# Kernel optimization log

Measured on AMD Instinct MI355X. Metric: run time of the kernel, lower is better.

The kernel has to match this reference:

```python
import jax, jax.numpy as jnp
import numpy as np

IMG = 8       # image_size
LH = 150      # l_h
LQ = 10       # l_q
K = 10        # value-iteration steps
B = 16384     # batch
N_STATES = 2 + IMG * IMG


def _conv(x, w, pad):
    # NCHW conv, stride 1
    return jax.lax.conv_general_dilated(
        x, w, window_strides=(1, 1), padding=[(pad, pad), (pad, pad)],
        dimension_numbers=('NCHW', 'OIHW', 'NCHW'))


def setup_inputs() -> dict:
    key = jax.random.key(0)
    ks = jax.random.split(key, 8)
    grid = jax.random.normal(ks[0], (B, IMG * IMG), dtype=jnp.float32)
    pos = jax.random.randint(ks[1], (B, 2), 0, IMG).astype(jnp.float32)
    S = jnp.concatenate([grid, pos], axis=1)                      # [B, 66]
    Wh = jax.random.normal(ks[2], (LH, 1, 3, 3), jnp.float32) * 0.1
    bh = jnp.zeros((LH,), jnp.float32)
    Wr = jax.random.normal(ks[3], (1, LH, 1, 1), jnp.float32) * 0.1
    Wq = jax.random.normal(ks[4], (LQ, 1, 3, 3), jnp.float32) * 0.1
    w = jax.random.normal(ks[5], (LQ, 1, 3, 3), jnp.float32) * 0.1
    Wfc = jax.random.normal(ks[6], (8, LQ), jnp.float32) * 0.1
    return {'S': S, 'Wh': Wh, 'bh': bh, 'Wr': Wr, 'Wq': Wq, 'w': w, 'Wfc': Wfc}


def reference(S, Wh, bh, Wr, Wq, w, Wfc):
    X = S[:, :IMG * IMG].reshape(-1, 1, IMG, IMG)                 # [B,1,8,8]
    s1 = S[:, IMG * IMG].astype(jnp.int32)                        # row index
    s2 = S[:, IMG * IMG + 1].astype(jnp.int32)                    # col index

    h = _conv(X, Wh, 1) + bh[None, :, None, None]                 # [B,150,8,8]
    r = _conv(h, Wr, 0)                                           # [B,1,8,8]
    q = _conv(r, Wq, 1)                                           # [B,10,8,8]
    v = jnp.max(q, axis=1, keepdims=True)                         # [B,1,8,8]

    Wcat = jnp.concatenate([Wq, w], axis=1)                       # [10,2,3,3]

    def step(v, _):
        qq = _conv(jnp.concatenate([r, v], axis=1), Wcat, 1)
        return jnp.max(qq, axis=1, keepdims=True), None

    v, _ = jax.lax.scan(step, v, None, length=K - 1)
    q = _conv(jnp.concatenate([r, v], axis=1), Wcat, 1)           # [B,10,8,8]

    bidx = jnp.arange(q.shape[0])
    q_sel = q[bidx, :, s1, s2]                                    # [B,10]
    logits = q_sel @ Wfc.T                                        # [B,8]
    return logits
```

## Files before the change

### kernel.cpp

```cpp
#include <hip/hip_runtime.h>

#define IMG 8
#define LH 150
#define LQ 10
#define KITER 10
#define ROW (IMG * IMG + 2)

__device__ __forceinline__ float bperm(int byte_addr, float v) {
    return __builtin_bit_cast(float,
        __builtin_amdgcn_ds_bpermute(byte_addr, __builtin_bit_cast(int, v)));
}

__device__ __forceinline__ float max10(const float q[LQ]) {
    const float g0 = fmaxf(fmaxf(q[0], q[1]), q[2]);
    const float g1 = fmaxf(fmaxf(q[3], q[4]), q[5]);
    const float g2 = fmaxf(fmaxf(q[6], q[7]), q[8]);
    return fmaxf(fmaxf(g0, g1), fmaxf(g2, q[9]));
}

__global__ void weff_kernel(const float* __restrict__ Wh,
                            const float* __restrict__ bh,
                            const float* __restrict__ Wr,
                            float* __restrict__ ws) {
    const int wv = threadIdx.x >> 6;
    const int lane = threadIdx.x & 63;
    float partial = 0.f;
    for (int c = lane; c < LH; c += 64) {
        const float wr = Wr[c];
        partial += wr * ((wv < 9) ? Wh[c * 9 + wv] : bh[c]);
    }
    #pragma unroll
    for (int off = 32; off > 0; off >>= 1)
        partial += __shfl_xor(partial, off);
    if (lane == 0) ws[wv] = partial;
}

__global__ __launch_bounds__(256, 2) void vin_kernel(
    const float* __restrict__ S,
    const float* __restrict__ Wq,
    const float* __restrict__ w,
    const float* __restrict__ Wfc,
    const float* __restrict__ ws,
    float* __restrict__ out,
    int B) {
    const int wave = threadIdx.x >> 6;
    const int lane = threadIdx.x & 63;
    const long b0 = (long)(blockIdx.x * 4 + wave) * 2;
    if (b0 >= B) return;

    const int y = lane >> 3, x = lane & 7;

    int   addr[9];
    float msk[9];
    #pragma unroll
    for (int t = 0; t < 9; ++t) {
        const int dy = t / 3 - 1, dx = t % 3 - 1;
        const int ny = y + dy, nx = x + dx;
        const bool v = ((unsigned)ny < 8u) && ((unsigned)nx < 8u);
        addr[t] = (v ? (ny * 8 + nx) : 0) << 2;
        msk[t]  = v ? 1.f : 0.f;
    }

    float wreg[LQ][9];
    #pragma unroll
    for (int o = 0; o < LQ; ++o)
        #pragma unroll
        for (int t = 0; t < 9; ++t)
            wreg[o][t] = w[o * 9 + t] * msk[t];

    const float* S0 = S + b0 * ROW;
    const float X0 = S0[lane];
    const float X1 = S0[ROW + lane];
    const int sel0 = ((int)S0[IMG * IMG] * 8 + (int)S0[IMG * IMG + 1]) << 2;
    const int sel1 = ((int)S0[ROW + IMG * IMG] * 8 + (int)S0[ROW + IMG * IMG + 1]) << 2;

    float r0 = ws[9], r1 = ws[9];
    #pragma unroll
    for (int t = 0; t < 9; ++t) {
        const float wm = ws[t] * msk[t];
        r0 = fmaf(wm, bperm(addr[t], X0), r0);
        r1 = fmaf(wm, bperm(addr[t], X1), r1);
    }

    float qr0[LQ], qr1[LQ];
    #pragma unroll
    for (int t = 0; t < 9; ++t) {
        const float a0 = bperm(addr[t], r0) * msk[t];
        const float a1 = bperm(addr[t], r1) * msk[t];
        #pragma unroll
        for (int o = 0; o < LQ; ++o) {
            const float wq = Wq[o * 9 + t];
            if (t == 0) { qr0[o] = a0 * wq; qr1[o] = a1 * wq; }
            else        { qr0[o] = fmaf(a0, wq, qr0[o]);
                          qr1[o] = fmaf(a1, wq, qr1[o]); }
        }
    }

    float v0 = max10(qr0), v1 = max10(qr1);

    #pragma unroll
    for (int k = 0; k < KITER - 1; ++k) {
        float vn0[9], vn1[9];
        #pragma unroll
        for (int t = 0; t < 9; ++t) {
            vn0[t] = bperm(addr[t], v0);
            vn1[t] = bperm(addr[t], v1);
        }
        float m0, m1;
        #pragma unroll
        for (int o = 0; o < LQ; ++o) {
            float acc0 = qr0[o], acc1 = qr1[o];
            #pragma unroll
            for (int t = 0; t < 9; ++t) {
                acc0 = fmaf(vn0[t], wreg[o][t], acc0);
                acc1 = fmaf(vn1[t], wreg[o][t], acc1);
            }
            if (o == 0) { m0 = acc0; m1 = acc1; }
            else        { m0 = fmaxf(m0, acc0); m1 = fmaxf(m1, acc1); }
        }
        v0 = m0; v1 = m1;
    }

    float qs0[LQ], qs1[LQ];
    {
        float vn0[9], vn1[9];
        #pragma unroll
        for (int t = 0; t < 9; ++t) {
            vn0[t] = bperm(addr[t], v0);
            vn1[t] = bperm(addr[t], v1);
        }
        #pragma unroll
        for (int o = 0; o < LQ; ++o) {
            float acc0 = qr0[o], acc1 = qr1[o];
            #pragma unroll
            for (int t = 0; t < 9; ++t) {
                acc0 = fmaf(vn0[t], wreg[o][t], acc0);
                acc1 = fmaf(vn1[t], wreg[o][t], acc1);
            }
            qs0[o] = bperm(sel0, acc0);
            qs1[o] = bperm(sel1, acc1);
        }
    }

    if (lane < 16) {
        const int row = lane & 7;
        float acc = 0.f;
        #pragma unroll
        for (int o = 0; o < LQ; ++o)
            acc = fmaf((lane < 8) ? qs0[o] : qs1[o], Wfc[row * LQ + o], acc);
        out[b0 * 8 + lane] = acc;
    }
}

extern "C" void kernel_launch(void* const* d_in, const int* in_sizes, int n_in,
                              void* d_out, int out_size, void* d_ws, size_t ws_size,
                              hipStream_t stream) {
    const float* S   = (const float*)d_in[0];
    const float* Wh  = (const float*)d_in[1];
    const float* bh  = (const float*)d_in[2];
    const float* Wr  = (const float*)d_in[3];
    const float* Wq  = (const float*)d_in[4];
    const float* w   = (const float*)d_in[5];
    const float* Wfc = (const float*)d_in[6];
    float* out = (float*)d_out;
    float* ws  = (float*)d_ws;

    const int B = in_sizes[0] / ROW;

    weff_kernel<<<1, 640, 0, stream>>>(Wh, bh, Wr, ws);

    const int grid = (B + 7) / 8;
    vin_kernel<<<grid, 256, 0, stream>>>(S, Wq, w, Wfc, ws, out, B);
}
```

Measured before the change: 94.99 us.

## Pack two samples into float2 FMAs and use DPP shifts for stencil neighbors

```diff
diff --git a/kernel.cpp b/kernel.cpp
--- a/kernel.cpp
+++ b/kernel.cpp
@@ -6,16 +6,44 @@
 #define KITER 10
 #define ROW (IMG * IMG + 2)
 
+typedef float f32x2 __attribute__((ext_vector_type(2)));
+
 __device__ __forceinline__ float bperm(int byte_addr, float v) {
     return __builtin_bit_cast(float,
         __builtin_amdgcn_ds_bpermute(byte_addr, __builtin_bit_cast(int, v)));
 }
 
-__device__ __forceinline__ float max10(const float q[LQ]) {
-    const float g0 = fmaxf(fmaxf(q[0], q[1]), q[2]);
-    const float g1 = fmaxf(fmaxf(q[3], q[4]), q[5]);
-    const float g2 = fmaxf(fmaxf(q[6], q[7]), q[8]);
-    return fmaxf(fmaxf(g0, g1), fmaxf(g2, q[9]));
+template <int CTRL>
+__device__ __forceinline__ float dppf(float v) {
+    return __builtin_bit_cast(float,
+        __builtin_amdgcn_update_dpp(0, __builtin_bit_cast(int, v),
+                                    CTRL, 0xF, 0xF, true));
+}
+#define DPP_SHR1 0x111
+#define DPP_SHL1 0x101
+
+__device__ __forceinline__ f32x2 fma2(f32x2 a, f32x2 b, f32x2 c) {
+#if __has_builtin(__builtin_elementwise_fma)
+    return __builtin_elementwise_fma(a, b, c);
+#else
+    return a * b + c;
+#endif
+}
+__device__ __forceinline__ f32x2 max2(f32x2 a, f32x2 b) {
+    f32x2 r; r.x = fmaxf(a.x, b.x); r.y = fmaxf(a.y, b.y); return r;
+}
+
+__device__ __forceinline__ void gather9(f32x2 vn[9], f32x2 v, int aU, int aD) {
+    f32x2 vU, vD;
+    vU.x = bperm(aU, v.x); vU.y = bperm(aU, v.y);
+    vD.x = bperm(aD, v.x); vD.y = bperm(aD, v.y);
+    vn[1] = vU; vn[4] = v; vn[7] = vD;
+    vn[0].x = dppf<DPP_SHR1>(vU.x); vn[0].y = dppf<DPP_SHR1>(vU.y);
+    vn[2].x = dppf<DPP_SHL1>(vU.x); vn[2].y = dppf<DPP_SHL1>(vU.y);
+    vn[3].x = dppf<DPP_SHR1>(v.x);  vn[3].y = dppf<DPP_SHR1>(v.y);
+    vn[5].x = dppf<DPP_SHL1>(v.x);  vn[5].y = dppf<DPP_SHL1>(v.y);
+    vn[6].x = dppf<DPP_SHR1>(vD.x); vn[6].y = dppf<DPP_SHR1>(vD.y);
+    vn[8].x = dppf<DPP_SHL1>(vD.x); vn[8].y = dppf<DPP_SHL1>(vD.y);
 }
 
 __global__ void weff_kernel(const float* __restrict__ Wh,
@@ -50,106 +78,96 @@
 
     const int y = lane >> 3, x = lane & 7;
 
-    int   addr[9];
     float msk[9];
     #pragma unroll
     for (int t = 0; t < 9; ++t) {
-        const int dy = t / 3 - 1, dx = t % 3 - 1;
-        const int ny = y + dy, nx = x + dx;
-        const bool v = ((unsigned)ny < 8u) && ((unsigned)nx < 8u);
-        addr[t] = (v ? (ny * 8 + nx) : 0) << 2;
-        msk[t]  = v ? 1.f : 0.f;
+        const int ny = y + t / 3 - 1, nx = x + t % 3 - 1;
+        msk[t] = (((unsigned)ny < 8u) && ((unsigned)nx < 8u)) ? 1.f : 0.f;
+    }
+    const int aU = ((y > 0) ? (lane - 8) : 0) << 2;
+    const int aD = ((y < 7) ? (lane + 8) : 0) << 2;
+
+    const float* S0 = S + b0 * ROW;
+    f32x2 X; X.x = S0[lane]; X.y = S0[ROW + lane];
+    const int sel0 = ((int)S0[IMG * IMG] * 8 + (int)S0[IMG * IMG + 1]) << 2;
+    const int sel1 = ((int)S0[ROW + IMG * IMG] * 8 + (int)S0[ROW + IMG * IMG + 1]) << 2;
+
+    f32x2 r;
+    {
+        f32x2 xn[9]; gather9(xn, X, aU, aD);
+        const float b = ws[9];
+        r.x = b; r.y = b;
+        #pragma unroll
+        for (int t = 0; t < 9; ++t) {
+            const float wm = ws[t] * msk[t];
+            f32x2 w2; w2.x = wm; w2.y = wm;
+            r = fma2(xn[t], w2, r);
+        }
     }
 
-    float wreg[LQ][9];
+    f32x2 qr[LQ];
+    {
+        f32x2 rn[9]; gather9(rn, r, aU, aD);
+        #pragma unroll
+        for (int t = 0; t < 9; ++t) {
+            f32x2 a; a.x = rn[t].x * msk[t]; a.y = rn[t].y * msk[t];
+            #pragma unroll
+            for (int o = 0; o < LQ; ++o) {
+                const float wq = Wq[o * 9 + t];
+                f32x2 w2; w2.x = wq; w2.y = wq;
+                qr[o] = (t == 0) ? (a * w2) : fma2(a, w2, qr[o]);
+            }
+        }
+    }
+
+    f32x2 wp[LQ][9];
     #pragma unroll
     for (int o = 0; o < LQ; ++o)
         #pragma unroll
-        for (int t = 0; t < 9; ++t)
-            wreg[o][t] = w[o * 9 + t] * msk[t];
+        for (int t = 0; t < 9; ++t) {
+            const float wm = w[o * 9 + t] * msk[t];
+            wp[o][t].x = wm; wp[o][t].y = wm;
+        }
 
-    const float* S0 = S + b0 * ROW;
-    const float X0 = S0[lane];
-    const float X1 = S0[ROW + lane];
-    const int sel0 = ((int)S0[IMG * IMG] * 8 + (int)S0[IMG * IMG + 1]) << 2;
-    const int sel1 = ((int)S0[ROW + IMG * IMG] * 8 + (int)S0[ROW + IMG * IMG + 1]) << 2;
-
-    float r0 = ws[9], r1 = ws[9];
-    #pragma unroll
-    for (int t = 0; t < 9; ++t) {
-        const float wm = ws[t] * msk[t];
-        r0 = fmaf(wm, bperm(addr[t], X0), r0);
-        r1 = fmaf(wm, bperm(addr[t], X1), r1);
+    f32x2 v;
+    {
+        const f32x2 g0 = max2(max2(qr[0], qr[1]), qr[2]);
+        const f32x2 g1 = max2(max2(qr[3], qr[4]), qr[5]);
+        const f32x2 g2 = max2(max2(qr[6], qr[7]), qr[8]);
+        v = max2(max2(g0, g1), max2(g2, qr[9]));
     }
-
-    float qr0[LQ], qr1[LQ];
-    #pragma unroll
-    for (int t = 0; t < 9; ++t) {
-        const float a0 = bperm(addr[t], r0) * msk[t];
-        const float a1 = bperm(addr[t], r1) * msk[t];
-        #pragma unroll
-        for (int o = 0; o < LQ; ++o) {
-            const float wq = Wq[o * 9 + t];
-            if (t == 0) { qr0[o] = a0 * wq; qr1[o] = a1 * wq; }
-            else        { qr0[o] = fmaf(a0, wq, qr0[o]);
-                          qr1[o] = fmaf(a1, wq, qr1[o]); }
-        }
-    }
-
-    float v0 = max10(qr0), v1 = max10(qr1);
 
     #pragma unroll
     for (int k = 0; k < KITER - 1; ++k) {
-        float vn0[9], vn1[9];
-        #pragma unroll
-        for (int t = 0; t < 9; ++t) {
-            vn0[t] = bperm(addr[t], v0);
-            vn1[t] = bperm(addr[t], v1);
-        }
-        float m0, m1;
+        f32x2 vn[9]; gather9(vn, v, aU, aD);
+        f32x2 m;
         #pragma unroll
         for (int o = 0; o < LQ; ++o) {
-            float acc0 = qr0[o], acc1 = qr1[o];
+            f32x2 acc = qr[o];
             #pragma unroll
-            for (int t = 0; t < 9; ++t) {
-                acc0 = fmaf(vn0[t], wreg[o][t], acc0);
-                acc1 = fmaf(vn1[t], wreg[o][t], acc1);
-            }
-            if (o == 0) { m0 = acc0; m1 = acc1; }
-            else        { m0 = fmaxf(m0, acc0); m1 = fmaxf(m1, acc1); }
+            for (int t = 0; t < 9; ++t)
+                acc = fma2(vn[t], wp[o][t], acc);
+            m = (o == 0) ? acc : max2(m, acc);
         }
-        v0 = m0; v1 = m1;
+        v = m;
     }
 
-    float qs0[LQ], qs1[LQ];
+    float oacc = 0.f;
     {
-        float vn0[9], vn1[9];
-        #pragma unroll
-        for (int t = 0; t < 9; ++t) {
-            vn0[t] = bperm(addr[t], v0);
-            vn1[t] = bperm(addr[t], v1);
-        }
+        f32x2 vn[9]; gather9(vn, v, aU, aD);
+        const int row = lane & 7;
         #pragma unroll
         for (int o = 0; o < LQ; ++o) {
-            float acc0 = qr0[o], acc1 = qr1[o];
+            f32x2 acc = qr[o];
             #pragma unroll
-            for (int t = 0; t < 9; ++t) {
-                acc0 = fmaf(vn0[t], wreg[o][t], acc0);
-                acc1 = fmaf(vn1[t], wreg[o][t], acc1);
-            }
-            qs0[o] = bperm(sel0, acc0);
-            qs1[o] = bperm(sel1, acc1);
+            for (int t = 0; t < 9; ++t)
+                acc = fma2(vn[t], wp[o][t], acc);
+            const float q0 = bperm(sel0, acc.x);
+            const float q1 = bperm(sel1, acc.y);
+            oacc = fmaf((lane < 8) ? q0 : q1, Wfc[row * LQ + o], oacc);
         }
     }
-
-    if (lane < 16) {
-        const int row = lane & 7;
-        float acc = 0.f;
-        #pragma unroll
-        for (int o = 0; o < LQ; ++o)
-            acc = fmaf((lane < 8) ? qs0[o] : qs1[o], Wfc[row * LQ + o], acc);
-        out[b0 * 8 + lane] = acc;
-    }
+    if (lane < 16) out[b0 * 8 + lane] = oacc;
 }
 
 extern "C" void kernel_launch(void* const* d_in, const int* in_sizes, int n_in,
```

Measured after the change: 91.83 us. 1.03x faster.
